# Kernel optimization log

Hardware: AMD Instinct MI355X
Metric: run time of the kernel (lower is better)

Reference implementation:

```python
import jax, jax.numpy as jnp
import numpy as np

N_NODES = 250000
N_EDGES = 4000000
NUM_FEATURES = 1
HIDDEN_DIM = 16
NUM_CLASSES = 4


def setup_inputs() -> dict:
    key = jax.random.key(0)
    ks = jax.random.split(key, 8)
    x = jax.random.normal(ks[0], (N_NODES, NUM_FEATURES), dtype=jnp.float32)
    edge_index = jax.random.randint(ks[1], (2, N_EDGES), 0, N_NODES, dtype=jnp.int64)
    # GCNConv weights: lin has no bias; bias added after aggregation
    W1 = jax.random.normal(ks[2], (NUM_FEATURES, HIDDEN_DIM), dtype=jnp.float32) * 0.5
    b1 = jax.random.normal(ks[3], (HIDDEN_DIM,), dtype=jnp.float32) * 0.1
    W2 = jax.random.normal(ks[4], (HIDDEN_DIM, HIDDEN_DIM), dtype=jnp.float32) * 0.25
    b2 = jax.random.normal(ks[5], (HIDDEN_DIM,), dtype=jnp.float32) * 0.1
    Wfc = jax.random.normal(ks[6], (HIDDEN_DIM, NUM_CLASSES), dtype=jnp.float32) * 0.25
    bfc = jax.random.normal(ks[7], (NUM_CLASSES,), dtype=jnp.float32) * 0.1
    return {"x": x, "edge_index": edge_index, "W1": W1, "b1": b1,
            "W2": W2, "b2": b2, "Wfc": Wfc, "bfc": bfc}


def _gcn_conv(x, row, col, norm, W, b, n):
    # x: [N, F_in]; row/col: [E'] (source/target incl self-loops); norm: [E']
    h = x @ W                                  # [N, F_out]
    msg = h[row] * norm[:, None]               # gather + scale, [E', F_out]
    out = jax.ops.segment_sum(msg, col, num_segments=n)  # scatter-add, [N, F_out]
    return out + b


def reference(x, edge_index, W1, b1, W2, b2, Wfc, bfc):
    n = x.shape[0]
    loops = jnp.arange(n, dtype=edge_index.dtype)
    row = jnp.concatenate([edge_index[0], loops])  # source nodes + self-loops
    col = jnp.concatenate([edge_index[1], loops])  # target nodes + self-loops
    # symmetric normalization: deg computed over targets (incl self-loops)
    deg = jax.ops.segment_sum(jnp.ones(col.shape, x.dtype), col, num_segments=n)
    dinv = jnp.where(deg > 0, jax.lax.rsqrt(deg), 0.0)
    norm = dinv[row] * dinv[col]                   # [E']
    h = jax.nn.relu(_gcn_conv(x, row, col, norm, W1, b1, n))
    h = jax.nn.relu(_gcn_conv(h, row, col, norm, W2, b2, n))
    return h @ Wfc + bfc
```

## Files before the change

### kernel.cpp

```cpp
#include <hip/hip_runtime.h>
#include <math.h>

#define HD 16
#define NC 4
#define BSH 8
#define BSZ 256
#define NSB 64
#define SBSH 12
#define CAP1 69632
#define CAP2 5120
#define S2 16
#define NFB 1024
#define NIV 17
#define STR 35
#define SMASK 0x3FFFFu

__global__ void k_thr(const float* __restrict__ W1, const float* __restrict__ b1,
                      float* __restrict__ ts, int* __restrict__ splits,
                      int* __restrict__ signs) {
    if (threadIdx.x != 0 || blockIdx.x != 0) return;
    float t[HD], s[HD];
    for (int f = 0; f < HD; ++f) {
        float w = W1[f];
        t[f] = (w != 0.0f) ? (-b1[f] / w) : INFINITY;
        s[f] = t[f];
    }
    for (int i = 1; i < HD; ++i) {
        float key = s[i]; int j = i - 1;
        while (j >= 0 && s[j] > key) { s[j + 1] = s[j]; --j; }
        s[j + 1] = key;
    }
    for (int f = 0; f < HD; ++f) ts[f] = s[f];
    for (int f = 0; f < HD; ++f) {
        float w = W1[f];
        if (w == 0.0f) { signs[f] = 0; splits[f] = 0; continue; }
        int c = 0;
        for (int g = 0; g < HD; ++g) c += (s[g] < t[f]) ? 1 : 0;
        splits[f] = c + 1;
        signs[f] = (w > 0.0f) ? 1 : -1;
    }
}

__global__ void k_part1(const int* __restrict__ row, const int* __restrict__ col,
                        int* __restrict__ cursor1, unsigned* __restrict__ bins1,
                        int E, int CHK) {
    __shared__ int hist[NSB];
    __shared__ int lbase[NSB];
    int t = threadIdx.x;
    int cb = blockIdx.x * CHK;
    int ce = min(E, cb + CHK);
    if (t < NSB) hist[t] = 0;
    __syncthreads();
    for (int e = cb + t; e < ce; e += blockDim.x)
        atomicAdd(&hist[col[e] >> SBSH], 1);
    __syncthreads();
    if (t < NSB) {
        int h = hist[t];
        lbase[t] = h ? atomicAdd(&cursor1[t * 16], h) : 0;
        hist[t] = 0;
    }
    __syncthreads();
    for (int e = cb + t; e < ce; e += blockDim.x) {
        int c = col[e];
        int sb = c >> SBSH;
        int pos = lbase[sb] + atomicAdd(&hist[sb], 1);
        if (pos < CAP1)
            bins1[(size_t)sb * CAP1 + pos] =
                (unsigned)row[e] | ((unsigned)(c & 4095) << 18);
    }
}

__global__ void k_part2(const unsigned* __restrict__ bins1, const int* __restrict__ cursor1,
                        int* __restrict__ cursor2, unsigned* __restrict__ bins2) {
    __shared__ int hist4[4][17];
    __shared__ int lbase[16];
    __shared__ int ofs[16];
    int t = threadIdx.x;
    int sb = blockIdx.x >> 4;
    int sp = blockIdx.x & 15;
    int cnt = cursor1[sb * 16];
    if (cnt > CAP1) cnt = CAP1;
    int s0 = sb * CAP1;
    int js = s0 + (int)(((long long)cnt * sp) / S2);
    int je = s0 + (int)(((long long)cnt * (sp + 1)) / S2);
    if (t < 16) { hist4[0][t] = 0; hist4[1][t] = 0; hist4[2][t] = 0; hist4[3][t] = 0; }
    __syncthreads();
    int cp = (t >> 4) & 3;
    for (int j = js + t; j < je; j += 256)
        atomicAdd(&hist4[cp][bins1[j] >> 26], 1);
    __syncthreads();
    if (t < 16) {
        int h = hist4[0][t] + hist4[1][t] + hist4[2][t] + hist4[3][t];
        lbase[t] = h ? atomicAdd(&cursor2[(sb * 16 + t) * 16], h) : 0;
        ofs[t] = 0;
    }
    __syncthreads();
    for (int j = js + t; j < je; j += 256) {
        unsigned rec = bins1[j];
        int fl = rec >> 26;
        int pos = lbase[fl] + atomicAdd(&ofs[fl], 1);
        if (pos < CAP2)
            bins2[(size_t)(sb * 16 + fl) * CAP2 + pos] =
                (rec & SMASK) | (((rec >> 18) & 255u) << 18);
    }
}

__global__ void k_degdx(const unsigned* __restrict__ bins, const int* __restrict__ cursor,
                        const float* __restrict__ x,
                        float* __restrict__ dinv, float* __restrict__ dx, int N) {
    __shared__ int cnt[BSZ];
    int t = threadIdx.x, b = blockIdx.x;
    cnt[t] = 0;
    __syncthreads();
    int m = cursor[b * 16];
    if (m > CAP2) m = CAP2;
    int s = b * CAP2, e = s + m;
    int full = ((e - s) >> 10) << 10;
    int ev = s + full;
    for (int j = s + (t << 2); j < ev; j += 1024) {
        uint4 rr = *reinterpret_cast<const uint4*>(bins + j);
        atomicAdd(&cnt[rr.x >> 18], 1);
        atomicAdd(&cnt[rr.y >> 18], 1);
        atomicAdd(&cnt[rr.z >> 18], 1);
        atomicAdd(&cnt[rr.w >> 18], 1);
    }
    for (int j = ev + t; j < e; j += 256) atomicAdd(&cnt[bins[j] >> 18], 1);
    __syncthreads();
    int node = (b << BSH) + t;
    if (node < N) {
        float d = rsqrtf((float)(cnt[t] + 1));
        dinv[node] = d;
        dx[node] = d * x[node];
    }
}

__global__ void k_s1(const unsigned* __restrict__ bins, const int* __restrict__ cursor,
                     const float* __restrict__ dinv, const float* __restrict__ dx,
                     const float* __restrict__ ts,
                     float2* __restrict__ gpq, int N) {
    __shared__ float sacc[BSZ];
    int t = threadIdx.x, b = blockIdx.x;
    sacc[t] = 0.0f;
    __syncthreads();
    int m = cursor[b * 16];
    if (m > CAP2) m = CAP2;
    int s = b * CAP2, e = s + m;
    int full = ((e - s) >> 10) << 10;
    int ev = s + full;
    for (int j = s + (t << 2); j < ev; j += 1024) {
        uint4 rr = *reinterpret_cast<const uint4*>(bins + j);
        float v0 = dx[rr.x & SMASK], v1 = dx[rr.y & SMASK],
              v2 = dx[rr.z & SMASK], v3 = dx[rr.w & SMASK];
        atomicAdd(&sacc[rr.x >> 18], v0);
        atomicAdd(&sacc[rr.y >> 18], v1);
        atomicAdd(&sacc[rr.z >> 18], v2);
        atomicAdd(&sacc[rr.w >> 18], v3);
    }
    for (int j = ev + t; j < e; j += 256) {
        unsigned r = bins[j];
        atomicAdd(&sacc[r >> 18], dx[r & SMASK]);
    }
    __syncthreads();
    int node = (b << BSH) + t;
    if (node < N) {
        float d = dinv[node];
        float S = d * (sacc[t] + dx[node]);
        int k = 0;
        #pragma unroll
        for (int g = 0; g < HD; ++g) k += (S > ts[g]);
        unsigned dq = (__float_as_uint(d) & ~31u) | (unsigned)k;
        gpq[node] = make_float2(d * S, __uint_as_float(dq));
    }
}

__global__ void __launch_bounds__(256, 1)
k_agg(const unsigned* __restrict__ bins, const int* __restrict__ cursor,
      const float2* __restrict__ gpq, const float* __restrict__ dinv,
      const int* __restrict__ splits, const int* __restrict__ signs,
      const float* __restrict__ W1, const float* __restrict__ b1,
      const float* __restrict__ W2, const float* __restrict__ b2,
      const float* __restrict__ Wfc, const float* __restrict__ bfc,
      float* __restrict__ out, int N) {
    __shared__ float acc[BSZ * STR];
    int t = threadIdx.x, b = blockIdx.x;
    for (int i = t; i < BSZ * STR; i += 256) acc[i] = 0.0f;
    __syncthreads();

    int m = cursor[b * 16];
    if (m > CAP2) m = CAP2;
    int s = b * CAP2, e = s + m;
    int full = ((e - s) >> 10) << 10;
    int ev = s + full;
    for (int j = s + (t << 2); j < ev; j += 1024) {
        uint4 rr = *reinterpret_cast<const uint4*>(bins + j);
        float2 p0 = gpq[rr.x & SMASK], p1 = gpq[rr.y & SMASK],
               p2 = gpq[rr.z & SMASK], p3 = gpq[rr.w & SMASK];
        float* a0 = &acc[(int)(rr.x >> 18) * STR + 2 * (int)(__float_as_uint(p0.y) & 31u)];
        float* a1 = &acc[(int)(rr.y >> 18) * STR + 2 * (int)(__float_as_uint(p1.y) & 31u)];
        float* a2 = &acc[(int)(rr.z >> 18) * STR + 2 * (int)(__float_as_uint(p2.y) & 31u)];
        float* a3 = &acc[(int)(rr.w >> 18) * STR + 2 * (int)(__float_as_uint(p3.y) & 31u)];
        atomicAdd(a0, p0.x); atomicAdd(a0 + 1, p0.y);
        atomicAdd(a1, p1.x); atomicAdd(a1 + 1, p1.y);
        atomicAdd(a2, p2.x); atomicAdd(a2 + 1, p2.y);
        atomicAdd(a3, p3.x); atomicAdd(a3 + 1, p3.y);
    }
    for (int j = ev + t; j < e; j += 256) {
        unsigned r = bins[j];
        float2 p = gpq[r & SMASK];
        float* a = &acc[(int)(r >> 18) * STR + 2 * (int)(__float_as_uint(p.y) & 31u)];
        atomicAdd(a, p.x); atomicAdd(a + 1, p.y);
    }
    __syncthreads();

    int node = (b << BSH) + t;
    if (node >= N) return;
    float Ppre[NIV + 1], Qpre[NIV + 1];
    float pp = 0.0f, qq = 0.0f;
    #pragma unroll
    for (int mm = 0; mm < NIV; ++mm) {
        Ppre[mm] = pp; Qpre[mm] = qq;
        pp += acc[t * STR + 2 * mm];
        qq += acc[t * STR + 2 * mm + 1];
    }
    Ppre[NIV] = pp; Qpre[NIV] = qq;

    float2 pq = gpq[node];
    float di = dinv[node];
    float si = pq.x / di;
    float aggv[HD];
    #pragma unroll
    for (int f = 0; f < HD; ++f) {
        int sp = splits[f], sg = signs[f];
        float w = W1[f], bb = b1[f];
        float A, B;
        if (sg > 0)      { A = pp - Ppre[sp]; B = qq - Qpre[sp]; }
        else if (sg < 0) { A = Ppre[sp];      B = Qpre[sp]; }
        else             { A = 0.0f;          B = (bb > 0.0f) ? qq : 0.0f; }
        float selfh = fmaxf(fmaf(w, si, bb), 0.0f);
        aggv[f] = di * (fmaf(w, A, bb * B) + di * selfh);
    }
    float o0 = bfc[0], o1 = bfc[1], o2 = bfc[2], o3 = bfc[3];
    #pragma unroll
    for (int f2 = 0; f2 < HD; ++f2) {
        float h = b2[f2];
        #pragma unroll
        for (int k = 0; k < HD; ++k) h = fmaf(aggv[k], W2[k * HD + f2], h);
        h = fmaxf(h, 0.0f);
        o0 = fmaf(h, Wfc[f2 * NC + 0], o0);
        o1 = fmaf(h, Wfc[f2 * NC + 1], o1);
        o2 = fmaf(h, Wfc[f2 * NC + 2], o2);
        o3 = fmaf(h, Wfc[f2 * NC + 3], o3);
    }
    ((float4*)out)[node] = make_float4(o0, o1, o2, o3);
}

extern "C" void kernel_launch(void* const* d_in, const int* in_sizes, int n_in,
                              void* d_out, int out_size, void* d_ws, size_t ws_size,
                              hipStream_t stream) {
    const float* x   = (const float*)d_in[0];
    const int*   ei  = (const int*)d_in[1];
    const float* W1  = (const float*)d_in[2];
    const float* b1  = (const float*)d_in[3];
    const float* W2  = (const float*)d_in[4];
    const float* b2  = (const float*)d_in[5];
    const float* Wfc = (const float*)d_in[6];
    const float* bfc = (const float*)d_in[7];
    float* out = (float*)d_out;

    const int N = in_sizes[0];
    const int E = in_sizes[1] / 2;
    const int* row = ei;
    const int* col = ei + E;

    char* ws = (char*)d_ws;
    size_t off = 0;
    unsigned* bins1 = (unsigned*)(ws + off); off += (size_t)NSB * CAP1 * 4;
    unsigned* bins2 = (unsigned*)(ws + off); off += (size_t)NFB * CAP2 * 4;
    int*    cursor1= (int*)(ws + off);   off += (size_t)NSB * 16 * 4;
    int*    cursor2= (int*)(ws + off);   off += (size_t)NFB * 16 * 4;
    float*  dinv  = (float*)(ws + off);  off += (size_t)N * 4;
    float*  dx    = (float*)(ws + off);  off += (size_t)N * 4;
    float2* gpq   = (float2*)(ws + off); off += (size_t)N * 8;
    float*  ts    = (float*)(ws + off);  off += 64;
    int*    splits= (int*)(ws + off);    off += 64;
    int*    signs = (int*)(ws + off);    off += 64;

    hipMemsetAsync(cursor1, 0, (size_t)(NSB + NFB) * 16 * 4, stream);

    const int B = 256;
    k_thr<<<1, 64, 0, stream>>>(W1, b1, ts, splits, signs);
    const int G1 = 1024;
    const int CHK = (E + G1 - 1) / G1;
    k_part1<<<G1, B, 0, stream>>>(row, col, cursor1, bins1, E, CHK);
    k_part2<<<NSB * S2, B, 0, stream>>>(bins1, cursor1, cursor2, bins2);
    k_degdx<<<NFB, B, 0, stream>>>(bins2, cursor2, x, dinv, dx, N);
    k_s1<<<NFB, B, 0, stream>>>(bins2, cursor2, dinv, dx, ts, gpq, N);
    k_agg<<<NFB, B, 0, stream>>>(bins2, cursor2, gpq, dinv, splits, signs,
                                 W1, b1, W2, b2, Wfc, bfc, out, N);
}
```

Measured before the change: 237.7 us.

## Fuse degree counting into partition pass and vectorize edge loads

Degree counting moves out of a separate pass over the binned edges and into the first partition kernel, which now does global atomicAdd on a per-node degree array while building its histogram. A simple elementwise kernel then computes dinv and dx from that array. The partition loops also load row and col as uint4, and the chunk size is rounded to a multiple of four to keep those loads aligned. The trade is 4M random global atomics plus an extra N-sized memset in exchange for dropping one full read of bins2 with shared-memory atomics.

```diff
diff --git a/kernel.cpp b/kernel.cpp
--- a/kernel.cpp
+++ b/kernel.cpp
@@ -42,17 +42,36 @@
 }
 
 __global__ void k_part1(const int* __restrict__ row, const int* __restrict__ col,
-                        int* __restrict__ cursor1, unsigned* __restrict__ bins1,
-                        int E, int CHK) {
+                        int* __restrict__ cursor1, int* __restrict__ deg,
+                        unsigned* __restrict__ bins1, int E, int CHK) {
     __shared__ int hist[NSB];
     __shared__ int lbase[NSB];
     int t = threadIdx.x;
     int cb = blockIdx.x * CHK;
     int ce = min(E, cb + CHK);
+    if (cb >= ce) return;
+    int n = ce - cb;
+    int nv = n >> 2;
+    const uint4* col4 = reinterpret_cast<const uint4*>(col + cb);
+    const uint4* row4 = reinterpret_cast<const uint4*>(row + cb);
     if (t < NSB) hist[t] = 0;
     __syncthreads();
-    for (int e = cb + t; e < ce; e += blockDim.x)
-        atomicAdd(&hist[col[e] >> SBSH], 1);
+    for (int i = t; i < nv; i += 256) {
+        uint4 c4 = col4[i];
+        atomicAdd(&hist[c4.x >> SBSH], 1);
+        atomicAdd(&hist[c4.y >> SBSH], 1);
+        atomicAdd(&hist[c4.z >> SBSH], 1);
+        atomicAdd(&hist[c4.w >> SBSH], 1);
+        atomicAdd(&deg[c4.x], 1);
+        atomicAdd(&deg[c4.y], 1);
+        atomicAdd(&deg[c4.z], 1);
+        atomicAdd(&deg[c4.w], 1);
+    }
+    for (int e = cb + (nv << 2) + t; e < ce; e += 256) {
+        int c = col[e];
+        atomicAdd(&hist[c >> SBSH], 1);
+        atomicAdd(&deg[c], 1);
+    }
     __syncthreads();
     if (t < NSB) {
         int h = hist[t];
@@ -60,13 +79,40 @@
         hist[t] = 0;
     }
     __syncthreads();
-    for (int e = cb + t; e < ce; e += blockDim.x) {
-        int c = col[e];
-        int sb = c >> SBSH;
+    for (int i = t; i < nv; i += 256) {
+        uint4 c4 = col4[i];
+        uint4 r4 = row4[i];
+        {
+            int sb = (int)(c4.x >> SBSH);
+            int pos = lbase[sb] + atomicAdd(&hist[sb], 1);
+            if (pos < CAP1)
+                bins1[(size_t)sb * CAP1 + pos] = r4.x | ((c4.x & 4095u) << 18);
+        }
+        {
+            int sb = (int)(c4.y >> SBSH);
+            int pos = lbase[sb] + atomicAdd(&hist[sb], 1);
+            if (pos < CAP1)
+                bins1[(size_t)sb * CAP1 + pos] = r4.y | ((c4.y & 4095u) << 18);
+        }
+        {
+            int sb = (int)(c4.z >> SBSH);
+            int pos = lbase[sb] + atomicAdd(&hist[sb], 1);
+            if (pos < CAP1)
+                bins1[(size_t)sb * CAP1 + pos] = r4.z | ((c4.z & 4095u) << 18);
+        }
+        {
+            int sb = (int)(c4.w >> SBSH);
+            int pos = lbase[sb] + atomicAdd(&hist[sb], 1);
+            if (pos < CAP1)
+                bins1[(size_t)sb * CAP1 + pos] = r4.w | ((c4.w & 4095u) << 18);
+        }
+    }
+    for (int e = cb + (nv << 2) + t; e < ce; e += 256) {
+        unsigned c = (unsigned)col[e];
+        int sb = (int)(c >> SBSH);
         int pos = lbase[sb] + atomicAdd(&hist[sb], 1);
         if (pos < CAP1)
-            bins1[(size_t)sb * CAP1 + pos] =
-                (unsigned)row[e] | ((unsigned)(c & 4095) << 18);
+            bins1[(size_t)sb * CAP1 + pos] = (unsigned)row[e] | ((c & 4095u) << 18);
     }
 }
 
@@ -105,32 +151,13 @@
     }
 }
 
-__global__ void k_degdx(const unsigned* __restrict__ bins, const int* __restrict__ cursor,
-                        const float* __restrict__ x,
-                        float* __restrict__ dinv, float* __restrict__ dx, int N) {
-    __shared__ int cnt[BSZ];
-    int t = threadIdx.x, b = blockIdx.x;
-    cnt[t] = 0;
-    __syncthreads();
-    int m = cursor[b * 16];
-    if (m > CAP2) m = CAP2;
-    int s = b * CAP2, e = s + m;
-    int full = ((e - s) >> 10) << 10;
-    int ev = s + full;
-    for (int j = s + (t << 2); j < ev; j += 1024) {
-        uint4 rr = *reinterpret_cast<const uint4*>(bins + j);
-        atomicAdd(&cnt[rr.x >> 18], 1);
-        atomicAdd(&cnt[rr.y >> 18], 1);
-        atomicAdd(&cnt[rr.z >> 18], 1);
-        atomicAdd(&cnt[rr.w >> 18], 1);
-    }
-    for (int j = ev + t; j < e; j += 256) atomicAdd(&cnt[bins[j] >> 18], 1);
-    __syncthreads();
-    int node = (b << BSH) + t;
-    if (node < N) {
-        float d = rsqrtf((float)(cnt[t] + 1));
-        dinv[node] = d;
-        dx[node] = d * x[node];
+__global__ void k_dinv(const int* __restrict__ deg, const float* __restrict__ x,
+                       float* __restrict__ dinv, float* __restrict__ dx, int N) {
+    int i = blockIdx.x * blockDim.x + threadIdx.x;
+    if (i < N) {
+        float d = rsqrtf((float)(deg[i] + 1));
+        dinv[i] = d;
+        dx[i] = d * x[i];
     }
 }
 
@@ -278,6 +305,7 @@
     unsigned* bins2 = (unsigned*)(ws + off); off += (size_t)NFB * CAP2 * 4;
     int*    cursor1= (int*)(ws + off);   off += (size_t)NSB * 16 * 4;
     int*    cursor2= (int*)(ws + off);   off += (size_t)NFB * 16 * 4;
+    int*    deg   = (int*)(ws + off);    off += (size_t)N * 4;
     float*  dinv  = (float*)(ws + off);  off += (size_t)N * 4;
     float*  dx    = (float*)(ws + off);  off += (size_t)N * 4;
     float2* gpq   = (float2*)(ws + off); off += (size_t)N * 8;
@@ -285,15 +313,16 @@
     int*    splits= (int*)(ws + off);    off += 64;
     int*    signs = (int*)(ws + off);    off += 64;
 
-    hipMemsetAsync(cursor1, 0, (size_t)(NSB + NFB) * 16 * 4, stream);
+    hipMemsetAsync(cursor1, 0, (size_t)(NSB + NFB) * 16 * 4 + (size_t)N * 4, stream);
 
     const int B = 256;
     k_thr<<<1, 64, 0, stream>>>(W1, b1, ts, splits, signs);
     const int G1 = 1024;
-    const int CHK = (E + G1 - 1) / G1;
-    k_part1<<<G1, B, 0, stream>>>(row, col, cursor1, bins1, E, CHK);
+    int CHK = (E + G1 - 1) / G1;
+    CHK = (CHK + 3) & ~3;
+    k_part1<<<G1, B, 0, stream>>>(row, col, cursor1, deg, bins1, E, CHK);
     k_part2<<<NSB * S2, B, 0, stream>>>(bins1, cursor1, cursor2, bins2);
-    k_degdx<<<NFB, B, 0, stream>>>(bins2, cursor2, x, dinv, dx, N);
+    k_dinv<<<(N + B - 1) / B, B, 0, stream>>>(deg, x, dinv, dx, N);
     k_s1<<<NFB, B, 0, stream>>>(bins2, cursor2, dinv, dx, ts, gpq, N);
     k_agg<<<NFB, B, 0, stream>>>(bins2, cursor2, gpq, dinv, splits, signs,
                                  W1, b1, W2, b2, Wfc, bfc, out, N);
```

Result: slower. 368.9 us (+55.2%).
